# Kernel tuning notes

Measured on AMD Instinct MI355X. Metric: run time of the kernel, lower is better.

Reference implementation:

```python
import jax, jax.numpy as jnp
import numpy as np

KS, PAD, N = 3, 1, 9  # deformable 3x3 kernel, padding 1, N = 9 taps
EPS = 1e-5


def conv2d(x, w, b=None, stride=1, padding=1):
    out = jax.lax.conv_general_dilated(
        x, w, (stride, stride), [(padding, padding)] * 2,
        dimension_numbers=("NCHW", "OIHW", "NCHW"))
    if b is not None:
        out = out + b[None, :, None, None]
    return out


def batchnorm(x, gamma, beta):
    # training-mode BN (fresh module, batch statistics), biased variance like torch
    mean = jnp.mean(x, axis=(0, 2, 3), keepdims=True)
    var = jnp.var(x, axis=(0, 2, 3), keepdims=True)
    xn = (x - mean) * jax.lax.rsqrt(var + EPS)
    return xn * gamma[None, :, None, None] + beta[None, :, None, None]


def gather_corners(xp, qx, qy):
    # xp: (b,c,Hp,Wp); qx,qy: (b,h,w,N) int32 -> (b,c,h,w,N)
    b, c, Hp, Wp = xp.shape
    _, h, w, n = qx.shape
    idx = (qx * Wp + qy).reshape(b, 1, h * w * n)
    out = jnp.take_along_axis(xp.reshape(b, c, Hp * Wp), idx, axis=2)
    return out.reshape(b, c, h, w, n)


def deform_conv(feat, offset, w4):
    # feat: (b,256,h,w), offset: (b,18,h,w) interleaved (x1,y1,x2,y2,...)
    b, c, h, w = feat.shape
    off_x = jnp.transpose(offset[:, 0::2], (0, 2, 3, 1))  # (b,h,w,N)
    off_y = jnp.transpose(offset[:, 1::2], (0, 2, 3, 1))
    xp = jnp.pad(feat, ((0, 0), (0, 0), (PAD, PAD), (PAD, PAD)))
    Hp, Wp = h + 2 * PAD, w + 2 * PAD
    # kernel tap offsets, row-major over (dx,dy)
    pn_x = jnp.array([-1, -1, -1, 0, 0, 0, 1, 1, 1], jnp.float32)
    pn_y = jnp.array([-1, 0, 1, -1, 0, 1, -1, 0, 1], jnp.float32)
    p0_x = jnp.arange(1, h + 1, dtype=jnp.float32)[None, :, None, None]
    p0_y = jnp.arange(1, w + 1, dtype=jnp.float32)[None, None, :, None]
    px = p0_x + pn_x[None, None, None, :] + off_x  # sampling coords in padded map
    py = p0_y + pn_y[None, None, None, :] + off_y

    fpx = jnp.floor(jax.lax.stop_gradient(px))
    fpy = jnp.floor(jax.lax.stop_gradient(py))
    q_lt_x = jnp.clip(fpx, 0, Hp - 1).astype(jnp.int32)
    q_lt_y = jnp.clip(fpy, 0, Wp - 1).astype(jnp.int32)
    q_rb_x = jnp.clip(fpx + 1, 0, Hp - 1).astype(jnp.int32)
    q_rb_y = jnp.clip(fpy + 1, 0, Wp - 1).astype(jnp.int32)

    # out-of-range points snapped to floor (as in original), then clamped
    mask_x = (px < PAD) | (px > Hp - 1 - PAD)
    mask_y = (py < PAD) | (py > Wp - 1 - PAD)
    px = jnp.clip(jnp.where(mask_x, jnp.floor(px), px), 0, Hp - 1)
    py = jnp.clip(jnp.where(mask_y, jnp.floor(py), py), 0, Wp - 1)

    ltx, lty = q_lt_x.astype(jnp.float32), q_lt_y.astype(jnp.float32)
    rbx, rby = q_rb_x.astype(jnp.float32), q_rb_y.astype(jnp.float32)
    g_lt = (1 + (ltx - px)) * (1 + (lty - py))
    g_rb = (1 - (rbx - px)) * (1 - (rby - py))
    g_lb = (1 + (ltx - px)) * (1 - (rby - py))
    g_rt = (1 - (rbx - px)) * (1 + (lty - py))

    x_off = (g_lt[:, None] * gather_corners(xp, q_lt_x, q_lt_y)
             + g_rb[:, None] * gather_corners(xp, q_rb_x, q_rb_y)
             + g_lb[:, None] * gather_corners(xp, q_lt_x, q_rb_y)
             + g_rt[:, None] * gather_corners(xp, q_rb_x, q_lt_y))  # (b,c,h,w,N)

    # stride-ks conv over the ks*ks-expanded map == contraction over (c, tap)
    outc = w4.shape[0]
    return jnp.einsum("bchwn,ocn->bohw", x_off, w4.reshape(outc, c, N))


def setup_inputs() -> dict:
    key = jax.random.key(0)
    ks = jax.random.split(key, 8)
    x = jax.random.normal(ks[0], (2, 3, 224, 224), jnp.float32)
    w1 = jax.random.normal(ks[1], (64, 3, 3, 3), jnp.float32) * 0.1
    b1 = jnp.zeros((64,), jnp.float32)
    g1 = jnp.ones((64,), jnp.float32)
    be1 = jnp.zeros((64,), jnp.float32)
    w2 = jax.random.normal(ks[2], (256, 64, 3, 3), jnp.float32) * 0.04
    b2 = jnp.zeros((256,), jnp.float32)
    g2 = jnp.ones((256,), jnp.float32)
    be2 = jnp.zeros((256,), jnp.float32)
    w_off = jax.random.normal(ks[3], (18, 256, 3, 3), jnp.float32) * 0.01
    b_off = jnp.zeros((18,), jnp.float32)
    w4 = jax.random.normal(ks[4], (256, 256, 3, 3), jnp.float32) * 0.02
    return dict(x=x, w1=w1, b1=b1, g1=g1, be1=be1, w2=w2, b2=b2, g2=g2,
                be2=be2, w_off=w_off, b_off=b_off, w4=w4)


def reference(x, w1, b1, g1, be1, w2, b2, g2, be2, w_off, b_off, w4):
    h = jax.nn.relu(conv2d(x, w1, b1))
    h = batchnorm(h, g1, be1)
    b_, c, H, W = h.shape
    h = h.reshape(b_, c, H // 2, 2, W // 2, 2).mean(axis=(3, 5))  # AvgPool 2x2
    h = jax.nn.relu(conv2d(h, w2, b2))
    h = batchnorm(h, g2, be2)
    offset = conv2d(h, w_off, b_off)  # (b,18,h,w)
    return deform_conv(h, offset, w4)
```

## Files before the change

### kernel.cpp

```cpp
#include <hip/hip_runtime.h>
#include <hip/hip_bf16.h>

#define NP1 50176
#define NP2 12544
#define NPP 12996

typedef __attribute__((ext_vector_type(8))) short short8;
typedef __attribute__((ext_vector_type(4))) float f32x4;

__device__ __forceinline__ unsigned short f2bu(float f){
  __hip_bfloat16 h = __float2bfloat16(f);
  return *reinterpret_cast<unsigned short*>(&h);
}
__device__ __forceinline__ float blo(unsigned u){ union{unsigned q; float f;} x; x.q = u<<16; return x.f; }
__device__ __forceinline__ float bhi(unsigned u){ union{unsigned q; float f;} x; x.q = u & 0xffff0000u; return x.f; }

#define S_SUM1   0
#define S_SUM2   128
#define S_STATS1 640
#define S_STATS2 768
#define S_WOFF2  1280
#define S_W4F    75008
#define S_W2FH   369920
#define S_W2FL   443648
#define S_OFFB   517376
#define S_PPAD   968960
#define S_PHI    2632448
#define S_PLO    3464192
#define S_HPAD   4295936
#define S_PBUF   10949888
#define S_HPADH  15014144
#define WS_NEED_FLOATS 18341120ull
#define WS_NEED_BYTES  (WS_NEED_FLOATS*4ull)

__global__ void k_w4f(const float* __restrict__ w4, unsigned short* __restrict__ w4f){
  int idx = blockIdx.x*256+threadIdx.x;
  int kt = idx/8192; int r = idx - kt*8192;
  int oc = r>>5, kk = r&31;
  int k = kt*32 + kk; int n = k>>8, c = k&255;
  w4f[idx] = f2bu(w4[oc*2304 + c*9 + n]);
}
__global__ void k_woff2(const float* __restrict__ woff, float* __restrict__ woff2){
  int idx = blockIdx.x*256+threadIdx.x;
  int k = idx>>5, oc = idx&31;
  int n = k>>8, c = k&255;
  woff2[idx] = (oc<18) ? woff[oc*2304 + c*9 + n] : 0.f;
}
__global__ void k_w2f(const float* __restrict__ w2, unsigned short* __restrict__ w2fh,
                      unsigned short* __restrict__ w2fl){
  int idx = blockIdx.x*256+threadIdx.x;
  int kt = idx/8192; int r = idx - kt*8192;
  int oc = r>>5, kk = r&31;
  int k = kt*32 + kk; int n = k>>6, c = k&63;
  float wv = w2[oc*576 + c*9 + n];
  unsigned short hi = f2bu(wv);
  w2fh[idx] = hi;
  w2fl[idx] = f2bu(wv - blo(hi));
}

__global__ __launch_bounds__(256) void k_conv1pool(
    const float* __restrict__ x, const float* __restrict__ w1, const float* __restrict__ b1,
    float* __restrict__ ppad, float* __restrict__ sum1){
  __shared__ float xs[3*34*34];
  int bid = blockIdx.x;
  int tile = bid % 49; int oc = (bid/49) & 63; int b = bid/(49*64);
  int tu = tile/7, tv = tile - 7*(tile/7);
  int tid = threadIdx.x;
  int in0 = tu*32 - 1, jn0 = tv*32 - 1;
  for(int t=tid; t<3468; t+=256){
    int c = t/1156; int r2 = t - c*1156; int rr = r2/34; int cc = r2 - rr*34;
    int ii = in0+rr, jj = jn0+cc;
    xs[t] = (ii>=0 && ii<224 && jj>=0 && jj<224) ? x[(size_t)(b*3+c)*NP1 + ii*224+jj] : 0.f;
  }
  float w[27];
  #pragma unroll
  for(int t=0;t<27;t++) w[t] = w1[oc*27+t];
  float bia = b1[oc];
  __syncthreads();
  int u = tid>>4, v = tid&15;
  float s1=0.f, s2=0.f, pl=0.f;
  #pragma unroll
  for(int dy=0;dy<2;dy++){
    #pragma unroll
    for(int dx=0;dx<2;dx++){
      float acc = bia;
      #pragma unroll
      for(int c=0;c<3;c++)
        #pragma unroll
        for(int kh=0;kh<3;kh++)
          #pragma unroll
          for(int kw=0;kw<3;kw++)
            acc += xs[c*1156 + (2*u+dy+kh)*34 + (2*v+dx+kw)] * w[c*9+kh*3+kw];
      acc = fmaxf(acc, 0.f);
      pl += acc; s1 += acc; s2 += acc*acc;
    }
  }
  int U = tu*16+u, V = tv*16+v;
  ppad[(size_t)(b*64+oc)*NPP + (U+1)*114 + (V+1)] = 0.25f*pl;
  __shared__ float r1[256], r2[256];
  r1[tid]=s1; r2[tid]=s2; __syncthreads();
  for(int o=128;o>0;o>>=1){
    if(tid<o){ r1[tid]+=r1[tid+o]; r2[tid]+=r2[tid+o]; }
    __syncthreads();
  }
  if(tid==0){ atomicAdd(&sum1[oc], r1[0]); atomicAdd(&sum1[64+oc], r2[0]); }
}

__global__ void k_fin1(const float* __restrict__ sum1, const float* __restrict__ g1,
                       const float* __restrict__ be1, float* __restrict__ stats1){
  int ch = threadIdx.x;
  float n = 2.f*(float)NP1;
  float mean = sum1[ch]/n;
  float var  = sum1[64+ch]/n - mean*mean;
  float sc = g1[ch]/sqrtf(var + 1e-5f);
  stats1[ch]    = sc;
  stats1[64+ch] = be1[ch] - mean*sc;
}

__global__ __launch_bounds__(256) void k_affine1t(const float* __restrict__ ppad,
        const float* __restrict__ stats1,
        unsigned short* __restrict__ phi, unsigned short* __restrict__ plo){
  __shared__ float ls[64*65];
  int bid = blockIdx.x;
  int b = bid/204; int pp0 = (bid - b*204)*64;
  int tid = threadIdx.x;
  #pragma unroll
  for(int it=0; it<16; it++){
    int t = it*256 + tid;
    int c = t>>6, q = t&63;
    int pp = pp0 + q;
    float v = 0.f;
    if(pp < NPP){
      int row = pp/114, col = pp - row*114;
      if(row>=1 && row<=112 && col>=1 && col<=112)
        v = stats1[c]*ppad[(size_t)(b*64+c)*NPP + pp] + stats1[64+c];
    }
    ls[c*65+q] = v;
  }
  __syncthreads();
  #pragma unroll
  for(int it=0; it<16; it++){
    int t = it*256 + tid;
    int q = t>>6, cq = t&63;
    int qq = t/64, c = t%64;
    (void)q; (void)cq;
    int pp = pp0 + qq%64;
    int qloc = qq & 63;
    pp = pp0 + qloc;
    if(pp < NPP){
      float v = ls[c*65 + qloc];
      unsigned short hi = f2bu(v);
      phi[((size_t)b*NPP + pp)*64 + c] = hi;
      plo[((size_t)b*NPP + pp)*64 + c] = f2bu(v - blo(hi));
    }
  }
}

__global__ __launch_bounds__(256) void k_conv2(
    const unsigned short* __restrict__ phi, const unsigned short* __restrict__ plo,
    const unsigned short* __restrict__ w2fh, const unsigned short* __restrict__ w2fl,
    const float* __restrict__ b2, float* __restrict__ hpad){
  __shared__ float smemf[8800];
  int*  pp_tbl = (int*)smemf;
  unsigned short* afh0 = (unsigned short*)(smemf + 576);
  unsigned short* afl0 = (unsigned short*)(smemf + 576 + 2560);
  float* tb = smemf + 576;
  const int tid = threadIdx.x;
  const int wave = tid>>6, lane = tid&63;
  const int sidx = (blockIdx.x & 7)*49 + (blockIdx.x >> 3);
  const int pix0 = sidx*64;
  const int b = pix0/NP2, ij0 = pix0 - b*NP2;

  for(int t=tid; t<576; t+=256){
    int p = t/9, n = t - 9*(t/9);
    int ij = ij0+p; int i = ij/112, j = ij - i*112;
    pp_tbl[p*9+n] = (i + n/3)*114 + (j + n%3);
  }
  const int px_g = tid>>2;
  const int coff = (tid&3)*8;
  const unsigned short* ph_b = phi + (size_t)b*NPP*64;
  const unsigned short* pl_b = plo + (size_t)b*NPP*64;

  f32x4 acc[4][4] = {};
  __syncthreads();

  auto STAGE = [&](int kt, int buf){
    int n = kt>>1; int cb = ((kt&1)<<5) + coff;
    int pp = pp_tbl[px_g*9 + n];
    *(uint4*)&afh0[buf*2560 + px_g*40 + coff] = *(const uint4*)(ph_b + (size_t)pp*64 + cb);
    *(uint4*)&afl0[buf*2560 + px_g*40 + coff] = *(const uint4*)(pl_b + (size_t)pp*64 + cb);
  };

  const int klo = (lane>>4)<<3;
  STAGE(0, 0);
  for(int kt=0; kt<18; kt++){
    __syncthreads();
    if(kt+1 < 18) STAGE(kt+1, (kt+1)&1);
    const unsigned short* abh = afh0 + (kt&1)*2560;
    const unsigned short* abl = afl0 + (kt&1)*2560;
    short8 aH[4], aL[4];
    #pragma unroll
    for(int mf=0; mf<4; mf++){
      aH[mf] = *(const short8*)&abh[(mf*16 + (lane&15))*40 + klo];
      aL[mf] = *(const short8*)&abl[(mf*16 + (lane&15))*40 + klo];
    }
    #pragma unroll
    for(int nf=0; nf<4; nf++){
      int oc = wave*64 + nf*16 + (lane&15);
      short8 bH = *(const short8*)&w2fh[(size_t)kt*8192 + oc*32 + klo];
      short8 bL = *(const short8*)&w2fl[(size_t)kt*8192 + oc*32 + klo];
      #pragma unroll
      for(int mf=0; mf<4; mf++){
        acc[mf][nf] = __builtin_amdgcn_mfma_f32_16x16x32_bf16(aH[mf], bH, acc[mf][nf], 0,0,0);
        acc[mf][nf] = __builtin_amdgcn_mfma_f32_16x16x32_bf16(aH[mf], bL, acc[mf][nf], 0,0,0);
        acc[mf][nf] = __builtin_amdgcn_mfma_f32_16x16x32_bf16(aL[mf], bH, acc[mf][nf], 0,0,0);
      }
    }
  }
  const int row0 = (lane>>4)<<2, col = lane&15;
  for(int half=0; half<2; half++){
    __syncthreads();
    #pragma unroll
    for(int m2=0; m2<2; m2++){
      int mf = half*2 + m2;
      #pragma unroll
      for(int nf=0; nf<4; nf++){
        int oc = wave*64 + nf*16 + col;
        #pragma unroll
        for(int r=0;r<4;r++) tb[(m2*16 + row0 + r)*257 + oc] = acc[mf][nf][r];
      }
    }
    __syncthreads();
    #pragma unroll
    for(int it=0; it<8; it++){
      int id = it*256 + tid;
      int pxl = id>>6, oc4 = id&63;
      int px = half*32 + pxl;
      int ij = ij0+px; int i = ij/112, j = ij - i*112;
      int pp = (i+1)*114 + (j+1);
      float4 v;
      v.x = fmaxf(tb[pxl*257 + oc4*4+0] + b2[oc4*4+0], 0.f);
      v.y = fmaxf(tb[pxl*257 + oc4*4+1] + b2[oc4*4+1], 0.f);
      v.z = fmaxf(tb[pxl*257 + oc4*4+2] + b2[oc4*4+2], 0.f);
      v.w = fmaxf(tb[pxl*257 + oc4*4+3] + b2[oc4*4+3], 0.f);
      *(float4*)&hpad[((size_t)b*NPP + pp)*256 + oc4*4] = v;
    }
  }
}

__global__ __launch_bounds__(256) void k_bnstats2(const float* __restrict__ hpad,
                                                  float* __restrict__ sum2){
  int c = threadIdx.x;
  int q0 = blockIdx.x*98;
  float s1=0.f, s2=0.f;
  for(int qi=0; qi<98; qi++){
    int q = q0+qi; int b = q/NP2; int pix = q - b*NP2;
    int pp = (pix/112 + 1)*114 + (pix%112) + 1;
    float v = hpad[((size_t)b*NPP + pp)*256 + c];
    s1 += v; s2 += v*v;
  }
  atomicAdd(&sum2[c], s1); atomicAdd(&sum2[256+c], s2);
}

__global__ void k_fin2(const float* __restrict__ sum2, const float* __restrict__ g2,
                       const float* __restrict__ be2, float* __restrict__ stats2){
  int ch = threadIdx.x;
  float n = 2.f*(float)NP2;
  float mean = sum2[ch]/n;
  float var  = sum2[256+ch]/n - mean*mean;
  float sc = g2[ch]/sqrtf(var + 1e-5f);
  stats2[ch]     = sc;
  stats2[256+ch] = be2[ch] - mean*sc;
}

__global__ void k_affine2(float* __restrict__ hpad, const float* __restrict__ stats2,
                          unsigned short* __restrict__ hpadh){
  int idx = blockIdx.x*256+threadIdx.x;
  int c = idx & 255; int pi = idx >> 8;
  int pp = pi % NPP;
  int row = pp/114, col = pp - row*114;
  bool in = (row>=1 && row<=112 && col>=1 && col<=112);
  float v = in ? (stats2[c]*hpad[idx] + stats2[256+c]) : 0.f;
  hpad[idx]  = v;
  hpadh[idx] = f2bu(v);
}

__global__ __launch_bounds__(256) void k_convoff_split(const float* __restrict__ hpad,
        const float* __restrict__ woff2, float* __restrict__ pbuf){
  __shared__ float Alds[32*65];
  __shared__ float Blds[1024];
  const int tid = threadIdx.x;
  const int xcd = blockIdx.x & 7;
  const int r   = blockIdx.x >> 3;
  const int n   = r/49;
  const int mt  = xcd*49 + (r - n*49);
  const int mbase = mt*64;
  const int b = mbase/NP2; const int ijbase = mbase - b*NP2;
  const int oc = tid & 31; const int p0 = (tid>>5)*8;
  const float* hb = hpad + (size_t)b*NPP*256;
  float acc[8] = {};
  for(int kt=0; kt<8; kt++){
    int c0 = kt*32;
    __syncthreads();
    ((float4*)Blds)[tid] = ((const float4*)(woff2 + ((size_t)n*256 + c0)*32))[tid];
    #pragma unroll
    for(int it=0; it<2; it++){
      int id = it*256+tid;
      int p = id>>3, kq = id&7;
      int ij = ijbase+p; int i = ij/112, j = ij - i*112;
      int pp = (i + n/3)*114 + j + (n%3);
      float4 v = *(const float4*)(hb + (size_t)pp*256 + c0 + kq*4);
      Alds[(kq*4+0)*65+p] = v.x;
      Alds[(kq*4+1)*65+p] = v.y;
      Alds[(kq*4+2)*65+p] = v.z;
      Alds[(kq*4+3)*65+p] = v.w;
    }
    __syncthreads();
    #pragma unroll
    for(int kk=0;kk<32;kk++){
      float bv = Blds[kk*32+oc];
      const float* ap = &Alds[kk*65+p0];
      #pragma unroll
      for(int i2=0;i2<8;i2++) acc[i2] = fmaf(ap[i2], bv, acc[i2]);
    }
  }
  if(oc<18){
    #pragma unroll
    for(int p=0;p<8;p++){
      int ij = ijbase+p0+p;
      pbuf[(size_t)n*451584 + ((size_t)(b*18+oc))*NP2 + ij] = acc[p];
    }
  }
}

__global__ void k_offred(const float* __restrict__ pbuf, const float* __restrict__ boff,
                         float* __restrict__ offb){
  int idx = blockIdx.x*256+threadIdx.x;
  int oc = (idx/NP2) % 18;
  float s = boff[oc];
  #pragma unroll
  for(int n=0;n<9;n++) s += pbuf[(size_t)n*451584 + idx];
  offb[idx] = s;
}

__global__ __launch_bounds__(256) void k_deform(
    const unsigned short* __restrict__ hpadh,
    const float* __restrict__ offb,
    const unsigned short* __restrict__ w4f,
    float* __restrict__ out){
  __shared__ int   gidx[64][9][4];
  __shared__ float gwt [64][9][4];
  __shared__ unsigned short afrag[2][64*40];
  const int tid = threadIdx.x;
  const int wave = tid>>6, lane = tid&63;
  const int sidx = (blockIdx.x & 7)*49 + (blockIdx.x >> 3);
  const int pix0 = sidx*64;
  const int b = pix0/NP2, ij0 = pix0 - b*NP2;

  for(int t=tid; t<576; t+=256){
    int p = t/9, n = t - 9*(t/9);
    int ij = ij0+p; int i = ij/112, j = ij - i*112;
    float ox = offb[(size_t)(b*18 + 2*n  )*NP2 + ij];
    float oy = offb[(size_t)(b*18 + 2*n+1)*NP2 + ij];
    float px = (float)(i + n/3) + ox;
    float py = (float)(j + n%3) + oy;
    float fpx = floorf(px), fpy = floorf(py);
    float qltxf = fminf(fmaxf(fpx,     0.f),113.f);
    float qltyf = fminf(fmaxf(fpy,     0.f),113.f);
    float qrbxf = fminf(fmaxf(fpx+1.f, 0.f),113.f);
    float qrbyf = fminf(fmaxf(fpy+1.f, 0.f),113.f);
    int qltx=(int)qltxf, qlty=(int)qltyf, qrbx=(int)qrbxf, qrby=(int)qrbyf;
    bool mx = (px<1.f)||(px>112.f);
    bool my = (py<1.f)||(py>112.f);
    float pxc = fminf(fmaxf(mx?fpx:px, 0.f),113.f);
    float pyc = fminf(fmaxf(my?fpy:py, 0.f),113.f);
    float glt = (1.f+(qltxf-pxc))*(1.f+(qltyf-pyc));
    float grb = (1.f-(qrbxf-pxc))*(1.f-(qrbyf-pyc));
    float glb = (1.f+(qltxf-pxc))*(1.f-(qrbyf-pyc));
    float grt = (1.f-(qrbxf-pxc))*(1.f+(qltyf-pyc));
    gidx[p][n][0]=qltx*114+qlty; gwt[p][n][0]=glt;
    gidx[p][n][1]=qrbx*114+qrby; gwt[p][n][1]=grb;
    gidx[p][n][2]=qltx*114+qrby; gwt[p][n][2]=glb;
    gidx[p][n][3]=qrbx*114+qlty; gwt[p][n][3]=grt;
  }

  const int px_g   = tid>>2;
  const int coff_g = (tid&3)*8;
  const unsigned short* hb = hpadh + (size_t)b*NPP*256;

  f32x4 acc[4][4] = {};
  __syncthreads();

  auto GATHER = [&](int kt, int buf){
    int n = kt>>3; int cb = ((kt&7)<<5) + coff_g;
    const int*   gi = gidx[px_g][n];
    const float* gw = gwt[px_g][n];
    f32x4 va = {0.f,0.f,0.f,0.f}, vb = {0.f,0.f,0.f,0.f};
    #pragma unroll
    for(int cr=0;cr<4;cr++){
      const uint4 u = *(const uint4*)(hb + (size_t)gi[cr]*256 + cb);
      float w = gw[cr];
      va.x = fmaf(w, blo(u.x), va.x); va.y = fmaf(w, bhi(u.x), va.y);
      va.z = fmaf(w, blo(u.y), va.z); va.w = fmaf(w, bhi(u.y), va.w);
      vb.x = fmaf(w, blo(u.z), vb.x); vb.y = fmaf(w, bhi(u.z), vb.y);
      vb.z = fmaf(w, blo(u.w), vb.z); vb.w = fmaf(w, bhi(u.w), vb.w);
    }
    uint4 o;
    o.x = (unsigned)f2bu(va.x) | ((unsigned)f2bu(va.y)<<16);
    o.y = (unsigned)f2bu(va.z) | ((unsigned)f2bu(va.w)<<16);
    o.z = (unsigned)f2bu(vb.x) | ((unsigned)f2bu(vb.y)<<16);
    o.w = (unsigned)f2bu(vb.z) | ((unsigned)f2bu(vb.w)<<16);
    *(uint4*)&afrag[buf][px_g*40 + coff_g] = o;
  };

  const int klo = (lane>>4)<<3;
  GATHER(0, 0);
  for(int kt=0; kt<72; kt++){
    __syncthreads();
    if(kt+1 < 72) GATHER(kt+1, (kt+1)&1);
    const unsigned short* ab = afrag[kt&1];
    short8 aF[4];
    #pragma unroll
    for(int mf=0; mf<4; mf++)
      aF[mf] = *(const short8*)&ab[(mf*16 + (lane&15))*40 + klo];
    const unsigned short* wb = w4f + (size_t)kt*8192 + klo;
    #pragma unroll
    for(int nf=0; nf<4; nf++){
      int oc = wave*64 + nf*16 + (lane&15);
      short8 bF = *(const short8*)&wb[oc*32];
      #pragma unroll
      for(int mf=0; mf<4; mf++)
        acc[mf][nf] = __builtin_amdgcn_mfma_f32_16x16x32_bf16(aF[mf], bF, acc[mf][nf], 0,0,0);
    }
  }
  int row0 = ((lane>>4)<<2);
  int col  = lane&15;
  #pragma unroll
  for(int mf=0; mf<4; mf++)
    #pragma unroll
    for(int nf=0; nf<4; nf++){
      int oc = wave*64 + nf*16 + col;
      size_t ob = (size_t)(b*256+oc)*NP2 + ij0 + mf*16 + row0;
      *(f32x4*)(out + ob) = acc[mf][nf];
    }
}

extern "C" void kernel_launch(void* const* d_in, const int* in_sizes, int n_in,
                              void* d_out, int out_size, void* d_ws, size_t ws_size,
                              hipStream_t stream){
  (void)in_sizes; (void)n_in;
  const float* x    = (const float*)d_in[0];
  const float* w1   = (const float*)d_in[1];
  const float* b1   = (const float*)d_in[2];
  const float* g1   = (const float*)d_in[3];
  const float* be1  = (const float*)d_in[4];
  const float* w2   = (const float*)d_in[5];
  const float* b2   = (const float*)d_in[6];
  const float* g2   = (const float*)d_in[7];
  const float* be2  = (const float*)d_in[8];
  const float* woff = (const float*)d_in[9];
  const float* boff = (const float*)d_in[10];
  const float* w4   = (const float*)d_in[11];
  float* out = (float*)d_out;
  float* ws = (float*)d_ws;

  if(ws_size < WS_NEED_BYTES){
    hipMemsetAsync(d_out, 0, (size_t)out_size*sizeof(float), stream);
    return;
  }

  float* sum1   = ws + S_SUM1;
  float* sum2   = ws + S_SUM2;
  float* stats1 = ws + S_STATS1;
  float* stats2 = ws + S_STATS2;
  float* woff2  = ws + S_WOFF2;
  unsigned short* w4f  = (unsigned short*)(ws + S_W4F);
  unsigned short* w2fh = (unsigned short*)(ws + S_W2FH);
  unsigned short* w2fl = (unsigned short*)(ws + S_W2FL);
  float* offb   = ws + S_OFFB;
  float* ppad   = ws + S_PPAD;
  unsigned short* phi = (unsigned short*)(ws + S_PHI);
  unsigned short* plo = (unsigned short*)(ws + S_PLO);
  float* hpad   = ws + S_HPAD;
  float* pbuf   = ws + S_PBUF;
  unsigned short* hpadh = (unsigned short*)(ws + S_HPADH);

  hipMemsetAsync(sum1, 0, 640*sizeof(float), stream);
  k_w4f          <<<2304,  256, 0, stream>>>(w4, w4f);
  k_woff2        <<<288,   256, 0, stream>>>(woff, woff2);
  k_w2f          <<<576,   256, 0, stream>>>(w2, w2fh, w2fl);
  k_conv1pool    <<<6272,  256, 0, stream>>>(x, w1, b1, ppad, sum1);
  k_fin1         <<<1,     64,  0, stream>>>(sum1, g1, be1, stats1);
  k_affine1t     <<<408,   256, 0, stream>>>(ppad, stats1, phi, plo);
  k_conv2        <<<392,   256, 0, stream>>>(phi, plo, w2fh, w2fl, b2, hpad);
  k_bnstats2     <<<256,   256, 0, stream>>>(hpad, sum2);
  k_fin2         <<<1,     256, 0, stream>>>(sum2, g2, be2, stats2);
  k_affine2      <<<25992, 256, 0, stream>>>(hpad, stats2, hpadh);
  k_convoff_split<<<3528,  256, 0, stream>>>(hpad, woff2, pbuf);
  k_offred       <<<1764,  256, 0, stream>>>(pbuf, boff, offb);
  k_deform       <<<392,   256, 0, stream>>>(hpadh, offb, w4f, out);
}
```

Baseline: 411.0 us.

## Compute offset conv with split-bf16 MFMA and fp32 fixup for boundary pixels

```diff
diff --git a/kernel.cpp b/kernel.cpp
--- a/kernel.cpp
+++ b/kernel.cpp
@@ -28,7 +28,9 @@
 #define S_PHI    2632448
 #define S_PLO    3464192
 #define S_HPAD   4295936
-#define S_PBUF   10949888
+#define S_HPADL  10949888
+#define S_WOFFH  14276864
+#define S_WOFFL  14313728
 #define S_HPADH  15014144
 #define WS_NEED_FLOATS 18341120ull
 #define WS_NEED_BYTES  (WS_NEED_FLOATS*4ull)
@@ -45,6 +47,17 @@
   int k = idx>>5, oc = idx&31;
   int n = k>>8, c = k&255;
   woff2[idx] = (oc<18) ? woff[oc*2304 + c*9 + n] : 0.f;
+}
+__global__ void k_wofff(const float* __restrict__ woff, unsigned short* __restrict__ woffh,
+                        unsigned short* __restrict__ woffl){
+  int idx = blockIdx.x*256+threadIdx.x;
+  int kt = idx>>10; int r = idx & 1023;
+  int oc = r>>5, kk = r&31;
+  int k = kt*32 + kk; int n = k>>8, c = k&255;
+  float wv = (oc<18) ? woff[oc*2304 + c*9 + n] : 0.f;
+  unsigned short hi = f2bu(wv);
+  woffh[idx] = hi;
+  woffl[idx] = f2bu(wv - blo(hi));
 }
 __global__ void k_w2f(const float* __restrict__ w2, unsigned short* __restrict__ w2fh,
                       unsigned short* __restrict__ w2fl){
@@ -274,7 +287,7 @@
 }
 
 __global__ void k_affine2(float* __restrict__ hpad, const float* __restrict__ stats2,
-                          unsigned short* __restrict__ hpadh){
+                          unsigned short* __restrict__ hpadh, unsigned short* __restrict__ hpadl){
   int idx = blockIdx.x*256+threadIdx.x;
   int c = idx & 255; int pi = idx >> 8;
   int pp = pi % NPP;
@@ -282,65 +295,108 @@
   bool in = (row>=1 && row<=112 && col>=1 && col<=112);
   float v = in ? (stats2[c]*hpad[idx] + stats2[256+c]) : 0.f;
   hpad[idx]  = v;
-  hpadh[idx] = f2bu(v);
-}
-
-__global__ __launch_bounds__(256) void k_convoff_split(const float* __restrict__ hpad,
-        const float* __restrict__ woff2, float* __restrict__ pbuf){
-  __shared__ float Alds[32*65];
-  __shared__ float Blds[1024];
+  unsigned short hi = f2bu(v);
+  hpadh[idx] = hi;
+  hpadl[idx] = f2bu(v - blo(hi));
+}
+
+__global__ __launch_bounds__(256) void k_convoff_mfma(
+    const unsigned short* __restrict__ hpadh, const unsigned short* __restrict__ hpadl,
+    const unsigned short* __restrict__ woffh, const unsigned short* __restrict__ woffl,
+    const float* __restrict__ boff, float* __restrict__ offb){
+  __shared__ int pp_tbl[576];
+  __shared__ unsigned short afh0[2*2560];
+  __shared__ unsigned short afl0[2*2560];
   const int tid = threadIdx.x;
-  const int xcd = blockIdx.x & 7;
-  const int r   = blockIdx.x >> 3;
-  const int n   = r/49;
-  const int mt  = xcd*49 + (r - n*49);
-  const int mbase = mt*64;
-  const int b = mbase/NP2; const int ijbase = mbase - b*NP2;
-  const int oc = tid & 31; const int p0 = (tid>>5)*8;
+  const int wave = tid>>6, lane = tid&63;
+  const int sidx = (blockIdx.x & 7)*49 + (blockIdx.x >> 3);
+  const int pix0 = sidx*64;
+  const int b = pix0/NP2, ij0 = pix0 - b*NP2;
+
+  for(int t=tid; t<576; t+=256){
+    int p = t/9, n = t - 9*(t/9);
+    int ij = ij0+p; int i = ij/112, j = ij - i*112;
+    pp_tbl[p*9+n] = (i + n/3)*114 + (j + n%3);
+  }
+  const int px_g = tid>>2;
+  const int coff = (tid&3)*8;
+  const unsigned short* ph_b = hpadh + (size_t)b*NPP*256;
+  const unsigned short* pl_b = hpadl + (size_t)b*NPP*256;
+
+  f32x4 acc[2] = {};
+  __syncthreads();
+
+  auto STAGE = [&](int kt, int buf){
+    int n = kt>>3; int cb = ((kt&7)<<5) + coff;
+    int pp = pp_tbl[px_g*9 + n];
+    *(uint4*)&afh0[buf*2560 + px_g*40 + coff] = *(const uint4*)(ph_b + (size_t)pp*256 + cb);
+    *(uint4*)&afl0[buf*2560 + px_g*40 + coff] = *(const uint4*)(pl_b + (size_t)pp*256 + cb);
+  };
+
+  const int klo = (lane>>4)<<3;
+  STAGE(0, 0);
+  for(int kt=0; kt<72; kt++){
+    __syncthreads();
+    if(kt+1 < 72) STAGE(kt+1, (kt+1)&1);
+    const unsigned short* abh = afh0 + (kt&1)*2560;
+    const unsigned short* abl = afl0 + (kt&1)*2560;
+    short8 aH = *(const short8*)&abh[(wave*16 + (lane&15))*40 + klo];
+    short8 aL = *(const short8*)&abl[(wave*16 + (lane&15))*40 + klo];
+    #pragma unroll
+    for(int nf=0; nf<2; nf++){
+      int oc = nf*16 + (lane&15);
+      short8 bH = *(const short8*)&woffh[(size_t)kt*1024 + oc*32 + klo];
+      short8 bL = *(const short8*)&woffl[(size_t)kt*1024 + oc*32 + klo];
+      acc[nf] = __builtin_amdgcn_mfma_f32_16x16x32_bf16(aH, bH, acc[nf], 0,0,0);
+      acc[nf] = __builtin_amdgcn_mfma_f32_16x16x32_bf16(aH, bL, acc[nf], 0,0,0);
+      acc[nf] = __builtin_amdgcn_mfma_f32_16x16x32_bf16(aL, bH, acc[nf], 0,0,0);
+    }
+  }
+  const int col = lane&15, row0 = (lane>>4)<<2;
+  const int px = wave*16 + row0;
+  #pragma unroll
+  for(int nf=0; nf<2; nf++){
+    int oc = nf*16 + col;
+    if(oc < 18){
+      float bia = boff[oc];
+      f32x4 v = acc[nf];
+      v.x += bia; v.y += bia; v.z += bia; v.w += bia;
+      *(f32x4*)(offb + (size_t)(b*18+oc)*NP2 + ij0 + px) = v;
+    }
+  }
+}
+
+__global__ __launch_bounds__(256) void k_offfix(const float* __restrict__ hpad,
+        const float* __restrict__ woff2, const float* __restrict__ boff,
+        float* __restrict__ offb){
+  int idx = blockIdx.x*256 + threadIdx.x;
+  if(idx >= 83712) return;
+  int oc = idx & 31;
+  int pid = idx >> 5;
+  int b = pid / 1308; int t = pid - b*1308;
+  int i, j;
+  if(t < 672){
+    int r = t/112; i = (r<3) ? r : 106+r; j = t - (t/112)*112;
+  } else {
+    int u = t - 672; i = 3 + u/6; int c6 = u - 6*(u/6);
+    j = (c6<3) ? c6 : 106+c6;
+  }
   const float* hb = hpad + (size_t)b*NPP*256;
-  float acc[8] = {};
-  for(int kt=0; kt<8; kt++){
-    int c0 = kt*32;
-    __syncthreads();
-    ((float4*)Blds)[tid] = ((const float4*)(woff2 + ((size_t)n*256 + c0)*32))[tid];
-    #pragma unroll
-    for(int it=0; it<2; it++){
-      int id = it*256+tid;
-      int p = id>>3, kq = id&7;
-      int ij = ijbase+p; int i = ij/112, j = ij - i*112;
-      int pp = (i + n/3)*114 + j + (n%3);
-      float4 v = *(const float4*)(hb + (size_t)pp*256 + c0 + kq*4);
-      Alds[(kq*4+0)*65+p] = v.x;
-      Alds[(kq*4+1)*65+p] = v.y;
-      Alds[(kq*4+2)*65+p] = v.z;
-      Alds[(kq*4+3)*65+p] = v.w;
-    }
-    __syncthreads();
-    #pragma unroll
-    for(int kk=0;kk<32;kk++){
-      float bv = Blds[kk*32+oc];
-      const float* ap = &Alds[kk*65+p0];
-      #pragma unroll
-      for(int i2=0;i2<8;i2++) acc[i2] = fmaf(ap[i2], bv, acc[i2]);
-    }
-  }
-  if(oc<18){
-    #pragma unroll
-    for(int p=0;p<8;p++){
-      int ij = ijbase+p0+p;
-      pbuf[(size_t)n*451584 + ((size_t)(b*18+oc))*NP2 + ij] = acc[p];
-    }
-  }
-}
-
-__global__ void k_offred(const float* __restrict__ pbuf, const float* __restrict__ boff,
-                         float* __restrict__ offb){
-  int idx = blockIdx.x*256+threadIdx.x;
-  int oc = (idx/NP2) % 18;
-  float s = boff[oc];
-  #pragma unroll
-  for(int n=0;n<9;n++) s += pbuf[(size_t)n*451584 + idx];
-  offb[idx] = s;
+  float acc = 0.f;
+  for(int n=0;n<9;n++){
+    const float* ap = hb + (size_t)((i + n/3)*114 + (j + n%3))*256;
+    const float* wp = woff2 + (size_t)n*256*32 + oc;
+    #pragma unroll 4
+    for(int c=0;c<256;c+=4){
+      float4 a = *(const float4*)(ap + c);
+      acc = fmaf(a.x, wp[(c+0)*32], acc);
+      acc = fmaf(a.y, wp[(c+1)*32], acc);
+      acc = fmaf(a.z, wp[(c+2)*32], acc);
+      acc = fmaf(a.w, wp[(c+3)*32], acc);
+    }
+  }
+  if(oc < 18)
+    offb[(size_t)(b*18+oc)*NP2 + i*112 + j] = acc + boff[oc];
 }
 
 __global__ __launch_bounds__(256) void k_deform(
@@ -474,20 +530,23 @@
   float* stats1 = ws + S_STATS1;
   float* stats2 = ws + S_STATS2;
   float* woff2  = ws + S_WOFF2;
-  unsigned short* w4f  = (unsigned short*)(ws + S_W4F);
-  unsigned short* w2fh = (unsigned short*)(ws + S_W2FH);
-  unsigned short* w2fl = (unsigned short*)(ws + S_W2FL);
+  unsigned short* w4f   = (unsigned short*)(ws + S_W4F);
+  unsigned short* w2fh  = (unsigned short*)(ws + S_W2FH);
+  unsigned short* w2fl  = (unsigned short*)(ws + S_W2FL);
+  unsigned short* woffh = (unsigned short*)(ws + S_WOFFH);
+  unsigned short* woffl = (unsigned short*)(ws + S_WOFFL);
   float* offb   = ws + S_OFFB;
   float* ppad   = ws + S_PPAD;
   unsigned short* phi = (unsigned short*)(ws + S_PHI);
   unsigned short* plo = (unsigned short*)(ws + S_PLO);
   float* hpad   = ws + S_HPAD;
-  float* pbuf   = ws + S_PBUF;
   unsigned short* hpadh = (unsigned short*)(ws + S_HPADH);
+  unsigned short* hpadl = (unsigned short*)(ws + S_HPADL);
 
   hipMemsetAsync(sum1, 0, 640*sizeof(float), stream);
   k_w4f          <<<2304,  256, 0, stream>>>(w4, w4f);
   k_woff2        <<<288,   256, 0, stream>>>(woff, woff2);
+  k_wofff        <<<288,   256, 0, stream>>>(woff, woffh, woffl);
   k_w2f          <<<576,   256, 0, stream>>>(w2, w2fh, w2fl);
   k_conv1pool    <<<6272,  256, 0, stream>>>(x, w1, b1, ppad, sum1);
   k_fin1         <<<1,     64,  0, stream>>>(sum1, g1, be1, stats1);
@@ -495,8 +554,8 @@
   k_conv2        <<<392,   256, 0, stream>>>(phi, plo, w2fh, w2fl, b2, hpad);
   k_bnstats2     <<<256,   256, 0, stream>>>(hpad, sum2);
   k_fin2         <<<1,     256, 0, stream>>>(sum2, g2, be2, stats2);
-  k_affine2      <<<25992, 256, 0, stream>>>(hpad, stats2, hpadh);
-  k_convoff_split<<<3528,  256, 0, stream>>>(hpad, woff2, pbuf);
-  k_offred       <<<1764,  256, 0, stream>>>(pbuf, boff, offb);
+  k_affine2      <<<25992, 256, 0, stream>>>(hpad, stats2, hpadh, hpadl);
+  k_convoff_mfma <<<392,   256, 0, stream>>>(hpadh, hpadl, woffh, woffl, boff, offb);
+  k_offfix       <<<327,   256, 0, stream>>>(hpad, woff2, boff, offb);
   k_deform       <<<392,   256, 0, stream>>>(hpadh, offb, w4f, out);
 }
```

New measurement: 424.1 us. 1.03x slower.
